# Optimization experiments

Measured on AMD Instinct MI355X. Metric: run time of the kernel, lower is better.

The kernel has to match this reference:

```python
import jax, jax.numpy as jnp
import numpy as np

B, T, H, NH = 2, 2048, 1024, 16
D = H // NH          # head dim = 64
K_CONV = 4           # short conv kernel size


def _dwconv_silu(x, w):
    # causal depthwise conv1d + silu; x:[B,T,C], w:[C,K]
    Kc = w.shape[1]
    xp = jnp.pad(x, ((0, 0), (Kc - 1, 0), (0, 0))).transpose(0, 2, 1)  # [B,C,T+K-1]
    y = jax.lax.conv_general_dilated(xp, w[:, None, :], (1,), 'VALID',
                                     feature_group_count=w.shape[0],
                                     dimension_numbers=('NCH', 'OIH', 'NCH'))
    return jax.nn.silu(y.transpose(0, 2, 1))


def _l2norm(x, eps=1e-6):
    return x * jax.lax.rsqrt(jnp.sum(x * x, -1, keepdims=True) + eps)


def _forward(hidden, Wq, Wk, Wv, conv_q, conv_k, conv_v, Wb, Wa, A_log, dt_bias, Wg, norm_w, Wo):
    Bh, Tt, Hh = hidden.shape
    nh = A_log.shape[0]
    d = Hh // nh
    q = _dwconv_silu(hidden @ Wq.T, conv_q).reshape(Bh, Tt, nh, d)
    k = _dwconv_silu(hidden @ Wk.T, conv_k).reshape(Bh, Tt, nh, d)
    v = _dwconv_silu(hidden @ Wv.T, conv_v).reshape(Bh, Tt, nh, d)
    q = _l2norm(q) * (d ** -0.5)
    k = _l2norm(k)
    beta = jax.nn.sigmoid(hidden @ Wb.T)                                  # [B,T,h]
    g = -jnp.exp(A_log) * jax.nn.softplus(hidden @ Wa.T + dt_bias)        # [B,T,h]

    def step(S, inp):
        qt, kt, vt, gt, bt = inp
        S = S * jnp.exp(gt)[..., None, None]                 # gated decay
        pred = jnp.einsum('bhk,bhkv->bhv', kt, S)            # current memory readout
        dv = (vt - pred) * bt[..., None]                     # delta-rule update
        S = S + jnp.einsum('bhk,bhv->bhkv', kt, dv)
        ot = jnp.einsum('bhk,bhkv->bhv', qt, S)
        return S, ot

    xs = (q.transpose(1, 0, 2, 3), k.transpose(1, 0, 2, 3), v.transpose(1, 0, 2, 3),
          g.transpose(1, 0, 2), beta.transpose(1, 0, 2))
    S0 = jnp.zeros((Bh, nh, d, d), hidden.dtype)
    _, o = jax.lax.scan(step, S0, xs)
    o = o.transpose(1, 0, 2, 3)                               # [B,T,h,d]
    gate = (hidden @ Wg.T).reshape(Bh, Tt, nh, d)
    o = o * jax.lax.rsqrt(jnp.mean(o * o, -1, keepdims=True) + 1e-5) * norm_w
    o = o * jax.nn.silu(gate)                                 # gated RMSNorm
    return o.reshape(Bh, Tt, Hh) @ Wo.T


def setup_inputs():
    key = jax.random.key(0)
    ks = jax.random.split(key, 16)
    s = 0.02
    return {
        'hidden': jax.random.normal(ks[0], (B, T, H), jnp.float32),
        'Wq': jax.random.normal(ks[1], (H, H), jnp.float32) * s,
        'Wk': jax.random.normal(ks[2], (H, H), jnp.float32) * s,
        'Wv': jax.random.normal(ks[3], (H, H), jnp.float32) * s,
        'conv_q': jax.random.normal(ks[4], (H, K_CONV), jnp.float32) * 0.5,
        'conv_k': jax.random.normal(ks[5], (H, K_CONV), jnp.float32) * 0.5,
        'conv_v': jax.random.normal(ks[6], (H, K_CONV), jnp.float32) * 0.5,
        'Wb': jax.random.normal(ks[7], (NH, H), jnp.float32) * s,
        'Wa': jax.random.normal(ks[8], (NH, H), jnp.float32) * s,
        'A_log': jnp.log(jax.random.uniform(ks[9], (NH,), jnp.float32, 1.0, 16.0)),
        'dt_bias': jnp.log(jnp.expm1(jax.random.uniform(ks[10], (NH,), jnp.float32, 1e-3, 0.1))),
        'Wg': jax.random.normal(ks[11], (H, H), jnp.float32) * s,
        'norm_w': jnp.ones((D,), jnp.float32),
        'Wo': jax.random.normal(ks[12], (H, H), jnp.float32) * s,
    }


def reference(hidden, Wq, Wk, Wv, conv_q, conv_k, conv_v, Wb, Wa, A_log, dt_bias, Wg, norm_w, Wo):
    return _forward(hidden, Wq, Wk, Wv, conv_q, conv_k, conv_v, Wb, Wa, A_log, dt_bias, Wg, norm_w, Wo)
```

## Files before the change

### kernel.cpp

```cpp
#include <hip/hip_runtime.h>
#include <hip/hip_bf16.h>

typedef unsigned short u16;
typedef __attribute__((ext_vector_type(4))) float f32x4;
typedef __attribute__((ext_vector_type(8))) short bf16x8;

#define TLEN 2048
#define NHEAD 16
#define HD 1024

__device__ inline u16 f2bf(float f) {
  unsigned x = __float_as_uint(f);
  return (u16)((x + 0x7fffu + ((x >> 16) & 1u)) >> 16);
}
__device__ inline float bf2f(u16 u) { return __uint_as_float(((unsigned)u) << 16); }

__device__ inline float wave_sum(float x) {
  x += __shfl_xor(x, 1);  x += __shfl_xor(x, 2);  x += __shfl_xor(x, 4);
  x += __shfl_xor(x, 8);  x += __shfl_xor(x, 16); x += __shfl_xor(x, 32);
  return x;
}

__device__ inline void storev(float* p, float v) { *p = v; }
__device__ inline void storev(u16* p, float v)   { *p = f2bf(v); }

__device__ inline int swz(int row, int col) {
  return (row << 7) + ((((col >> 3) ^ (row & 7)) << 4)) + ((col & 7) << 1);
}
__device__ inline bf16x8 frag(const u16* base, int row, int kslot) {
  return *(const bf16x8*)((const char*)base + (row << 7) +
                          (((kslot ^ (row & 7)) << 4)));
}

__global__ __launch_bounds__(256) void cvt_all(
    const float* __restrict__ h,  const float* __restrict__ wq,
    const float* __restrict__ wk, const float* __restrict__ wv,
    const float* __restrict__ wg, const float* __restrict__ wo,
    const float* __restrict__ Wb, const float* __restrict__ Wa,
    u16* __restrict__ dh,  u16* __restrict__ dhlo,
    u16* __restrict__ dwq, u16* __restrict__ dwk,
    u16* __restrict__ dwv, u16* __restrict__ dwg, u16* __restrict__ dwo,
    u16* __restrict__ dwba_h, u16* __restrict__ dwba_l) {
  const int b = blockIdx.x;
  if (b < 4096) {
    const size_t i = (size_t)b * 256 + threadIdx.x;
    float4 v = *(const float4*)(h + i * 4);
    ushort4 hi, lo;
    hi.x = f2bf(v.x); lo.x = f2bf(v.x - bf2f(hi.x));
    hi.y = f2bf(v.y); lo.y = f2bf(v.y - bf2f(hi.y));
    hi.z = f2bf(v.z); lo.z = f2bf(v.z - bf2f(hi.z));
    hi.w = f2bf(v.w); lo.w = f2bf(v.w - bf2f(hi.w));
    *(ushort4*)(dh + i * 4) = hi;
    *(ushort4*)(dhlo + i * 4) = lo;
  } else if (b < 9216) {
    const int wsel = (b - 4096) >> 10;
    const size_t i = (size_t)((b - 4096) & 1023) * 256 + threadIdx.x;
    const float* s; u16* d;
    switch (wsel) {
      case 0: s = wq; d = dwq; break;
      case 1: s = wk; d = dwk; break;
      case 2: s = wv; d = dwv; break;
      case 3: s = wg; d = dwg; break;
      default: s = wo; d = dwo; break;
    }
    float4 v = *(const float4*)(s + i * 4);
    ushort4 u;
    u.x = f2bf(v.x); u.y = f2bf(v.y); u.z = f2bf(v.z); u.w = f2bf(v.w);
    *(ushort4*)(d + i * 4) = u;
  } else {
    const size_t i = (size_t)(b - 9216) * 256 + threadIdx.x;
    const size_t flat = i * 4;
    const float* src = (flat < 16384) ? (Wb + flat) : (Wa + (flat - 16384));
    float4 v = *(const float4*)src;
    ushort4 hi, lo;
    hi.x = f2bf(v.x); lo.x = f2bf(v.x - bf2f(hi.x));
    hi.y = f2bf(v.y); lo.y = f2bf(v.y - bf2f(hi.y));
    hi.z = f2bf(v.z); lo.z = f2bf(v.z - bf2f(hi.z));
    hi.w = f2bf(v.w); lo.w = f2bf(v.w - bf2f(hi.w));
    *(ushort4*)(dwba_h + flat) = hi;
    *(ushort4*)(dwba_l + flat) = lo;
  }
}

__global__ __launch_bounds__(256, 2) void gemm_big(
    const u16* __restrict__ A,
    const u16* __restrict__ W0p, const u16* __restrict__ W1p,
    const u16* __restrict__ W2p, const u16* __restrict__ W3p,
    u16* __restrict__ C0, u16* __restrict__ C1,
    u16* __restrict__ C2, u16* __restrict__ C3,
    int M, int N, int K) {
  const u16* W; u16* C;
  switch (blockIdx.z) {
    case 0: W = W0p; C = C0; break;
    case 1: W = W1p; C = C1; break;
    case 2: W = W2p; C = C2; break;
    default: W = W3p; C = C3; break;
  }
  const int tid = threadIdx.x;
  const int lane = tid & 63, wid = tid >> 6;
  const int fr = lane & 15, fq = lane >> 4;
  const int row0 = blockIdx.y * 256, col0 = blockIdx.x * 128;
  __shared__ __align__(16) u16 As[256 * 64];
  __shared__ __align__(16) u16 Bs[128 * 64];

  const u16* aSrc[8]; const u16* bSrc[4];
#pragma unroll
  for (int it = 0; it < 8; ++it) {
    const int s = it * 256 + tid;
    const int r = s >> 3, cc = s & 7;
    aSrc[it] = A + (size_t)(row0 + r) * K + (cc ^ (r & 7)) * 8;
  }
#pragma unroll
  for (int it = 0; it < 4; ++it) {
    const int s = it * 256 + tid;
    const int r = s >> 3, cc = s & 7;
    bSrc[it] = W + (size_t)(col0 + r) * K + (cc ^ (r & 7)) * 8;
  }
  int aOff[4][2], bOff[8][2];
#pragma unroll
  for (int m = 0; m < 4; ++m)
#pragma unroll
    for (int kk = 0; kk < 2; ++kk) {
      const int ra = wid * 64 + m * 16 + fr;
      aOff[m][kk] = ra * 128 + ((((kk << 2) | fq) ^ (ra & 7)) << 4);
    }
#pragma unroll
  for (int n = 0; n < 8; ++n)
#pragma unroll
    for (int kk = 0; kk < 2; ++kk) {
      const int rb = n * 16 + fr;
      bOff[n][kk] = rb * 128 + ((((kk << 2) | fq) ^ (rb & 7)) << 4);
    }

  f32x4 acc[4][8] = {};
  for (int k0 = 0; k0 < K; k0 += 64) {
#pragma unroll
    for (int it = 0; it < 8; ++it)
      __builtin_amdgcn_global_load_lds(
          (const __attribute__((address_space(1))) void*)(aSrc[it] + k0),
          (__attribute__((address_space(3))) void*)((char*)As + (it * 256 + tid) * 16),
          16, 0, 0);
#pragma unroll
    for (int it = 0; it < 4; ++it)
      __builtin_amdgcn_global_load_lds(
          (const __attribute__((address_space(1))) void*)(bSrc[it] + k0),
          (__attribute__((address_space(3))) void*)((char*)Bs + (it * 256 + tid) * 16),
          16, 0, 0);
    __syncthreads();
#pragma unroll
    for (int kk = 0; kk < 2; ++kk) {
      bf16x8 af[4], bfr[8];
#pragma unroll
      for (int m = 0; m < 4; ++m)
        af[m] = *(const bf16x8*)((const char*)As + aOff[m][kk]);
#pragma unroll
      for (int n = 0; n < 8; ++n)
        bfr[n] = *(const bf16x8*)((const char*)Bs + bOff[n][kk]);
#pragma unroll
      for (int m = 0; m < 4; ++m)
#pragma unroll
        for (int n = 0; n < 8; ++n)
          acc[m][n] = __builtin_amdgcn_mfma_f32_16x16x32_bf16(af[m], bfr[n], acc[m][n], 0, 0, 0);
    }
    __syncthreads();
  }
#pragma unroll
  for (int m = 0; m < 4; ++m)
#pragma unroll
    for (int n = 0; n < 8; ++n)
#pragma unroll
      for (int r = 0; r < 4; ++r) {
        const int gr = row0 + wid * 64 + m * 16 + fq * 4 + r;
        const int gc = col0 + n * 16 + fr;
        C[(size_t)gr * N + gc] = f2bf(acc[m][n][r]);
      }
}

template <typename OutT, int MT>
__global__ __launch_bounds__(256) void gemm_lin(
    const u16* __restrict__ A, const u16* __restrict__ W,
    OutT* __restrict__ C, int M, int N, int K) {
  const int tid = threadIdx.x;
  const int lane = tid & 63, wid = tid >> 6;
  const int wr = wid >> 1, wc = wid & 1;
  const int fr = lane & 15, fq = lane >> 4;
  const int row0 = blockIdx.y * (MT * 32), col0 = blockIdx.x * 128;
  __shared__ __align__(16) u16 As[MT * 32 * 64];
  __shared__ __align__(16) u16 Bs[128 * 64];

  const u16* aSrc[MT]; const u16* bSrc[4];
#pragma unroll
  for (int it = 0; it < MT; ++it) {
    const int c = it * 256 + tid;
    const int r = c >> 3, cc = c & 7, sc = cc ^ (r & 7);
    aSrc[it] = A + (size_t)(row0 + r) * K + sc * 8;
  }
#pragma unroll
  for (int it = 0; it < 4; ++it) {
    const int c = it * 256 + tid;
    const int r = c >> 3, cc = c & 7, sc = cc ^ (r & 7);
    bSrc[it] = W + (size_t)(col0 + r) * K + sc * 8;
  }
  int aOff[MT][2], bOff[4][2];
#pragma unroll
  for (int m = 0; m < MT; ++m)
#pragma unroll
    for (int kk = 0; kk < 2; ++kk) {
      const int ra = wr * (MT * 16) + m * 16 + fr;
      aOff[m][kk] = ra * 128 + ((((kk << 2) | fq) ^ (fr & 7)) << 4);
    }
#pragma unroll
  for (int n = 0; n < 4; ++n)
#pragma unroll
    for (int kk = 0; kk < 2; ++kk) {
      const int rb = wc * 64 + n * 16 + fr;
      bOff[n][kk] = rb * 128 + ((((kk << 2) | fq) ^ (fr & 7)) << 4);
    }

  f32x4 acc[MT][4] = {};
  for (int k0 = 0; k0 < K; k0 += 64) {
#pragma unroll
    for (int it = 0; it < MT; ++it)
      __builtin_amdgcn_global_load_lds(
          (const __attribute__((address_space(1))) void*)(aSrc[it] + k0),
          (__attribute__((address_space(3))) void*)((char*)As + (it * 256 + wid * 64) * 16),
          16, 0, 0);
#pragma unroll
    for (int it = 0; it < 4; ++it)
      __builtin_amdgcn_global_load_lds(
          (const __attribute__((address_space(1))) void*)(bSrc[it] + k0),
          (__attribute__((address_space(3))) void*)((char*)Bs + (it * 256 + wid * 64) * 16),
          16, 0, 0);
    __syncthreads();
#pragma unroll
    for (int kk = 0; kk < 2; ++kk) {
      bf16x8 af[MT], bfr[4];
#pragma unroll
      for (int m = 0; m < MT; ++m)
        af[m] = *(const bf16x8*)((const char*)As + aOff[m][kk]);
#pragma unroll
      for (int n = 0; n < 4; ++n)
        bfr[n] = *(const bf16x8*)((const char*)Bs + bOff[n][kk]);
#pragma unroll
      for (int m = 0; m < MT; ++m)
#pragma unroll
        for (int n = 0; n < 4; ++n)
          acc[m][n] = __builtin_amdgcn_mfma_f32_16x16x32_bf16(af[m], bfr[n], acc[m][n], 0, 0, 0);
    }
    __syncthreads();
  }
#pragma unroll
  for (int m = 0; m < MT; ++m)
#pragma unroll
    for (int n = 0; n < 4; ++n)
#pragma unroll
      for (int r = 0; r < 4; ++r) {
        const int gr = row0 + wr * (MT * 16) + m * 16 + fq * 4 + r;
        const int gc = col0 + wc * 64 + n * 16 + fr;
        storev(&C[(size_t)gr * N + gc], acc[m][n][r]);
      }
}

__global__ __launch_bounds__(256) void small_mfma(
    const u16* __restrict__ hhi, const u16* __restrict__ hlo,
    const u16* __restrict__ whi, const u16* __restrict__ wlo,
    const float* __restrict__ A_log, const float* __restrict__ dtb,
    float* __restrict__ bbuf, float* __restrict__ gbuf) {
  extern __shared__ char smc[];
  u16* Ahi = (u16*)smc;
  u16* Alo = (u16*)(smc + 32768);
  float* Red = (float*)(smc + 65536);
  const int tid = threadIdx.x;
  const int row0 = blockIdx.x * 16;
#pragma unroll
  for (int i = 0; i < 8; ++i) {
    const int slot = tid + 256 * i;
    const int r = slot >> 7, s = slot & 127;
    const int ss = s ^ (r & 7);
    const size_t src = (size_t)(row0 + r) * 1024 + (size_t)ss * 8;
    __builtin_amdgcn_global_load_lds(
        (const __attribute__((address_space(1))) void*)(hhi + src),
        (__attribute__((address_space(3))) void*)(Ahi + (size_t)slot * 8), 16, 0, 0);
    __builtin_amdgcn_global_load_lds(
        (const __attribute__((address_space(1))) void*)(hlo + src),
        (__attribute__((address_space(3))) void*)(Alo + (size_t)slot * 8), 16, 0, 0);
  }
  __syncthreads();
  const int w = tid >> 6, lane = tid & 63, fr = lane & 15, fq = lane >> 4;
  f32x4 acc[2] = {};
#pragma unroll
  for (int kk = 0; kk < 8; ++kk) {
    const int s = w * 32 + kk * 4 + fq;
    const size_t k = (size_t)w * 256 + kk * 32 + fq * 8;
    const int aoff = ((fr << 7) + (s ^ (fr & 7))) * 8;
    bf16x8 ah = *(const bf16x8*)(Ahi + aoff);
    bf16x8 al = *(const bf16x8*)(Alo + aoff);
#pragma unroll
    for (int ct = 0; ct < 2; ++ct) {
      const size_t boff = (size_t)(ct * 16 + fr) * 1024 + k;
      bf16x8 bh = *(const bf16x8*)(whi + boff);
      bf16x8 bl = *(const bf16x8*)(wlo + boff);
      acc[ct] = __builtin_amdgcn_mfma_f32_16x16x32_bf16(ah, bh, acc[ct], 0, 0, 0);
      acc[ct] = __builtin_amdgcn_mfma_f32_16x16x32_bf16(ah, bl, acc[ct], 0, 0, 0);
      acc[ct] = __builtin_amdgcn_mfma_f32_16x16x32_bf16(al, bh, acc[ct], 0, 0, 0);
    }
  }
#pragma unroll
  for (int ct = 0; ct < 2; ++ct)
#pragma unroll
    for (int rr = 0; rr < 4; ++rr)
      Red[(w * 16 + fq * 4 + rr) * 33 + ct * 16 + fr] = acc[ct][rr];
  __syncthreads();
  if (tid < 128) {
    const int row = tid >> 3, cg = (tid & 7) * 4;
#pragma unroll
    for (int j = 0; j < 4; ++j) {
      const int col = cg + j;
      const float s = Red[(0 * 16 + row) * 33 + col] + Red[(1 * 16 + row) * 33 + col]
                    + Red[(2 * 16 + row) * 33 + col] + Red[(3 * 16 + row) * 33 + col];
      const int grow = row0 + row;
      if (col < 16) {
        bbuf[grow * NHEAD + col] = 1.f / (1.f + __expf(-s));
      } else {
        const int hh = col - 16;
        const float xs = s + dtb[hh];
        const float sp = (xs > 20.f) ? xs : log1pf(__expf(xs));
        gbuf[grow * NHEAD + hh] = -__expf(A_log[hh]) * sp;
      }
    }
  }
}

__global__ __launch_bounds__(256) void chunk_local(
    const u16* __restrict__ qp, const u16* __restrict__ kp, const u16* __restrict__ vp,
    const float* __restrict__ cq, const float* __restrict__ ck, const float* __restrict__ cv,
    const float* __restrict__ gbuf, const float* __restrict__ bbuf,
    float* __restrict__ Pg, u16* __restrict__ Ug,
    u16* __restrict__ Rg, u16* __restrict__ Yg) {
  __shared__ __align__(16) u16 Kb[64 * 64];
  __shared__ __align__(16) u16 Qb[64 * 64];
  __shared__ __align__(16) u16 K2T[64 * 64];
  __shared__ __align__(16) u16 KWt[64 * 64];
  __shared__ __align__(16) u16 Vt[64 * 64];
  __shared__ __align__(16) u16 Zb[64 * 64];
  __shared__ __align__(16) u16 Zt[64 * 64];
  __shared__ __align__(16) u16 Mb[64 * 72];
  __shared__ __align__(16) float Cb[16 * 64];
  __shared__ float bcs[64], bet[64], e2v[64], Bv[64];
  u16* WTh = Mb;
  u16* uTh = KWt;
  u16* Gb  = Vt;

  const int bid = blockIdx.x;
  const int c = bid & 31, bh = bid >> 5;
  const int b = bh >> 4, h = bh & 15;
  const int tid = threadIdx.x;

  {
    int* zp = (int*)Zt;
#pragma unroll
    for (int i = 0; i < 8; ++i) zp[tid + 256 * i] = 0;
  }
  if (tid < 64) {
    const size_t gi = (size_t)((b * TLEN + c * 64) + tid) * NHEAD + h;
    bet[tid] = bbuf[gi];
    float v = gbuf[gi];
#pragma unroll
    for (int ofs = 1; ofs < 64; ofs <<= 1) {
      float tt = __shfl_up(v, ofs);
      if (tid >= ofs) v += tt;
    }
    bcs[tid] = v;
  }
  __syncthreads();
  if (tid < 64) {
    const float blast = bcs[63];
    Bv[tid]  = __expf(bcs[tid]);
    e2v[tid] = __expf(blast - bcs[tid]);
  }
  __syncthreads();

  {
    const int dq = (tid & 15) * 4;
    const int col = h * 64 + dq;
    float4 wq4[4], wk4[4], wv4[4];
#pragma unroll
    for (int jj = 0; jj < 4; ++jj) {
      wq4[jj] = *(const float4*)(cq + (size_t)(col + jj) * 4);
      wk4[jj] = *(const float4*)(ck + (size_t)(col + jj) * 4);
      wv4[jj] = *(const float4*)(cv + (size_t)(col + jj) * 4);
    }
#pragma unroll
    for (int i = 0; i < 4; ++i) {
      const int r = i * 16 + (tid >> 4);
      const int tcur = c * 64 + r;
      ushort4 xq[4], xk[4], xv[4];
#pragma unroll
      for (int m = 0; m < 4; ++m) {
        const int tt = tcur - 3 + m;
        if (tt >= 0) {
          const size_t a = (size_t)(b * TLEN + tt) * HD + col;
          xq[m] = *(const ushort4*)(qp + a);
          xk[m] = *(const ushort4*)(kp + a);
          xv[m] = *(const ushort4*)(vp + a);
        } else {
          xq[m] = ushort4{0, 0, 0, 0}; xk[m] = xq[m]; xv[m] = xq[m];
        }
      }
      float yq[4], yk[4], yv[4];
      float ssq = 0.f, ssk = 0.f;
#pragma unroll
      for (int jj = 0; jj < 4; ++jj) {
        float aq = wq4[jj].x * bf2f(((const u16*)&xq[0])[jj]) +
                   wq4[jj].y * bf2f(((const u16*)&xq[1])[jj]) +
                   wq4[jj].z * bf2f(((const u16*)&xq[2])[jj]) +
                   wq4[jj].w * bf2f(((const u16*)&xq[3])[jj]);
        float ak = wk4[jj].x * bf2f(((const u16*)&xk[0])[jj]) +
                   wk4[jj].y * bf2f(((const u16*)&xk[1])[jj]) +
                   wk4[jj].z * bf2f(((const u16*)&xk[2])[jj]) +
                   wk4[jj].w * bf2f(((const u16*)&xk[3])[jj]);
        float av = wv4[jj].x * bf2f(((const u16*)&xv[0])[jj]) +
                   wv4[jj].y * bf2f(((const u16*)&xv[1])[jj]) +
                   wv4[jj].z * bf2f(((const u16*)&xv[2])[jj]) +
                   wv4[jj].w * bf2f(((const u16*)&xv[3])[jj]);
        yq[jj] = aq / (1.f + __expf(-aq));
        yk[jj] = ak / (1.f + __expf(-ak));
        yv[jj] = av / (1.f + __expf(-av));
        ssq += yq[jj] * yq[jj];
        ssk += yk[jj] * yk[jj];
      }
      ssq += __shfl_xor(ssq, 1); ssq += __shfl_xor(ssq, 2);
      ssq += __shfl_xor(ssq, 4); ssq += __shfl_xor(ssq, 8);
      ssk += __shfl_xor(ssk, 1); ssk += __shfl_xor(ssk, 2);
      ssk += __shfl_xor(ssk, 4); ssk += __shfl_xor(ssk, 8);
      const float qsc = rsqrtf(ssq + 1e-6f) * 0.125f;
      const float ksc = rsqrtf(ssk + 1e-6f);
      const float bR = bet[r], e2R = e2v[r], wscR = bR * Bv[r];
      ushort4 qo, ko;
      float kvf[4];
#pragma unroll
      for (int jj = 0; jj < 4; ++jj) kvf[jj] = yk[jj] * ksc;
      qo.x = f2bf(yq[0] * qsc); qo.y = f2bf(yq[1] * qsc);
      qo.z = f2bf(yq[2] * qsc); qo.w = f2bf(yq[3] * qsc);
      ko.x = f2bf(kvf[0]); ko.y = f2bf(kvf[1]);
      ko.z = f2bf(kvf[2]); ko.w = f2bf(kvf[3]);
      *(ushort4*)((char*)Qb + swz(r, dq)) = qo;
      *(ushort4*)((char*)Kb + swz(r, dq)) = ko;
#pragma unroll
      for (int jj = 0; jj < 4; ++jj) {
        *(u16*)((char*)K2T + swz(dq + jj, r)) = f2bf(kvf[jj] * e2R);
        *(u16*)((char*)KWt + swz(dq + jj, r)) = f2bf(kvf[jj] * wscR);
        *(u16*)((char*)Vt  + swz(dq + jj, r)) = f2bf(yv[jj] * bR);
      }
    }
  }
  __syncthreads();

  const int w = tid >> 6, lane = tid & 63, fr = lane & 15, fq = lane >> 4;
  {
    bf16x8 ka0 = frag(Kb, w * 16 + fr, fq);
    bf16x8 ka1 = frag(Kb, w * 16 + fr, 4 + fq);
#pragma unroll
    for (int tc = 0; tc < 4; ++tc) {
      bf16x8 kb0 = frag(Kb, tc * 16 + fr, fq);
      bf16x8 kb1 = frag(Kb, tc * 16 + fr, 4 + fq);
      f32x4 a = {};
      a = __builtin_amdgcn_mfma_f32_16x16x32_bf16(ka0, kb0, a, 0, 0, 0);
      a = __builtin_amdgcn_mfma_f32_16x16x32_bf16(ka1, kb1, a, 0, 0, 0);
#pragma unroll
      for (int rr = 0; rr < 4; ++rr) {
        const int t = w * 16 + fq * 4 + rr, s = tc * 16 + fr;
        const float mv = (s < t) ? bet[t] * __expf(bcs[t] - bcs[s]) * a[rr] : 0.f;
        Mb[t * 72 + s] = f2bf(mv);
      }
    }
  }
  __syncthreads();

#pragma unroll 1
  for (int bi = 0; bi < 4; ++bi) {
    {
      const char* mrow = (const char*)Mb + (size_t)(bi * 16 + fr) * 144;
      bf16x8 ma0 = *(const bf16x8*)(mrow + fq * 16);
      bf16x8 ma1 = *(const bf16x8*)(mrow + 64 + fq * 16);
      bf16x8 zt0 = frag(Zt, w * 16 + fr, fq);
      bf16x8 zt1 = frag(Zt, w * 16 + fr, 4 + fq);
      f32x4 a = {};
      a = __builtin_amdgcn_mfma_f32_16x16x32_bf16(ma0, zt0, a, 0, 0, 0);
      a = __builtin_amdgcn_mfma_f32_16x16x32_bf16(ma1, zt1, a, 0, 0, 0);
#pragma unroll
      for (int rr = 0; rr < 4; ++rr)
        Cb[(fq * 4 + rr) * 64 + w * 16 + fr] = a[rr];
    }
    __syncthreads();
    if (tid < 64) {
      const int j = tid;
      float z[16];
#pragma unroll
      for (int t = 0; t < 16; ++t) {
        float acc = ((bi * 16 + t) == j ? 1.f : 0.f) - Cb[t * 64 + j];
        const u16* mrow = Mb + (size_t)(bi * 16 + t) * 72 + bi * 16;
#pragma unroll
        for (int s = 0; s < t; ++s) acc -= bf2f(mrow[s]) * z[s];
        z[t] = acc;
      }
#pragma unroll
      for (int t = 0; t < 16; ++t)
        *(u16*)((char*)Zb + swz(bi * 16 + t, j)) = f2bf(z[t]);
#pragma unroll
      for (int t4 = 0; t4 < 4; ++t4) {
        ushort4 zz;
        zz.x = f2bf(z[t4 * 4 + 0]); zz.y = f2bf(z[t4 * 4 + 1]);
        zz.z = f2bf(z[t4 * 4 + 2]); zz.w = f2bf(z[t4 * 4 + 3]);
        *(ushort4*)((char*)Zt + swz(j, bi * 16 + t4 * 4)) = zz;
      }
    }
    __syncthreads();
  }

  f32x4 accW[4], accu[4], accG[4];
  {
    bf16x8 kw0 = frag(KWt, w * 16 + fr, fq), kw1 = frag(KWt, w * 16 + fr, 4 + fq);
    bf16x8 vt0 = frag(Vt,  w * 16 + fr, fq), vt1 = frag(Vt,  w * 16 + fr, 4 + fq);
    bf16x8 qa0 = frag(Qb,  w * 16 + fr, fq), qa1 = frag(Qb,  w * 16 + fr, 4 + fq);
#pragma unroll
    for (int tc = 0; tc < 4; ++tc) {
      bf16x8 z0 = frag(Zb, tc * 16 + fr, fq), z1 = frag(Zb, tc * 16 + fr, 4 + fq);
      bf16x8 kb0 = frag(Kb, tc * 16 + fr, fq), kb1 = frag(Kb, tc * 16 + fr, 4 + fq);
      f32x4 aw = {}, au = {}, ag = {};
      aw = __builtin_amdgcn_mfma_f32_16x16x32_bf16(kw0, z0, aw, 0, 0, 0);
      aw = __builtin_amdgcn_mfma_f32_16x16x32_bf16(kw1, z1, aw, 0, 0, 0);
      au = __builtin_amdgcn_mfma_f32_16x16x32_bf16(vt0, z0, au, 0, 0, 0);
      au = __builtin_amdgcn_mfma_f32_16x16x32_bf16(vt1, z1, au, 0, 0, 0);
      ag = __builtin_amdgcn_mfma_f32_16x16x32_bf16(qa0, kb0, ag, 0, 0, 0);
      ag = __builtin_amdgcn_mfma_f32_16x16x32_bf16(qa1, kb1, ag, 0, 0, 0);
      accW[tc] = aw; accu[tc] = au; accG[tc] = ag;
    }
  }
  __syncthreads();
#pragma unroll
  for (int tc = 0; tc < 4; ++tc)
#pragma unroll
    for (int rr = 0; rr < 4; ++rr) {
      const int ro = w * 16 + fq * 4 + rr, co = tc * 16 + fr;
      *(u16*)((char*)WTh + swz(ro, co)) = f2bf(accW[tc][rr]);
      *(u16*)((char*)uTh + swz(ro, co)) = f2bf(accu[tc][rr]);
      const float gv = (co <= ro) ? accG[tc][rr] * __expf(bcs[ro] - bcs[co]) : 0.f;
      *(u16*)((char*)Gb + swz(ro, co)) = f2bf(gv);
    }
  __syncthreads();

  {
    bf16x8 k20 = frag(K2T, w * 16 + fr, fq), k21 = frag(K2T, w * 16 + fr, 4 + fq);
    bf16x8 g0  = frag(Gb,  w * 16 + fr, fq), g1  = frag(Gb,  w * 16 + fr, 4 + fq);
    const float bl = Bv[63];
    const size_t off = (size_t)bid * 4096;
#pragma unroll
    for (int tc = 0; tc < 4; ++tc) {
      bf16x8 w0 = frag(WTh, tc * 16 + fr, fq), w1 = frag(WTh, tc * 16 + fr, 4 + fq);
      bf16x8 u0 = frag(uTh, tc * 16 + fr, fq), u1 = frag(uTh, tc * 16 + fr, 4 + fq);
      f32x4 aP = {}, aU = {}, aR = {}, aY = {};
      aP = __builtin_amdgcn_mfma_f32_16x16x32_bf16(k20, w0, aP, 0, 0, 0);
      aP = __builtin_amdgcn_mfma_f32_16x16x32_bf16(k21, w1, aP, 0, 0, 0);
      aU = __builtin_amdgcn_mfma_f32_16x16x32_bf16(k20, u0, aU, 0, 0, 0);
      aU = __builtin_amdgcn_mfma_f32_16x16x32_bf16(k21, u1, aU, 0, 0, 0);
      aR = __builtin_amdgcn_mfma_f32_16x16x32_bf16(g0, w0, aR, 0, 0, 0);
      aR = __builtin_amdgcn_mfma_f32_16x16x32_bf16(g1, w1, aR, 0, 0, 0);
      aY = __builtin_amdgcn_mfma_f32_16x16x32_bf16(g0, u0, aY, 0, 0, 0);
      aY = __builtin_amdgcn_mfma_f32_16x16x32_bf16(g1, u1, aY, 0, 0, 0);
#pragma unroll
      for (int rr = 0; rr < 4; ++rr) {
        const int ar = w * 16 + fq * 4 + rr, cb = tc * 16 + fr;
        Pg[off + ar * 64 + cb] = ((ar == cb) ? bl : 0.f) - aP[rr];
        Ug[off + ar * 64 + cb] = f2bf(aU[rr]);
        const float qv = bf2f(*(const u16*)((const char*)Qb + swz(ar, cb)));
        Rg[off + ar * 64 + cb] = f2bf(Bv[ar] * qv - aR[rr]);
        Yg[off + ar * 64 + cb] = f2bf(aY[rr]);
      }
    }
  }
}

__global__ __launch_bounds__(256) void state_step(
    const float* __restrict__ Pg, const u16* __restrict__ Ug,
    u16* __restrict__ Sst) {
  __shared__ float Ps[64 * 65];
  __shared__ float Sc[64 * 20];
  const int blk = blockIdx.x;
  const int bh = blk >> 2, j0 = (blk & 3) * 16;
  const int tid = threadIdx.x;
  const int a = tid >> 2, jb = (tid & 3) * 4;
  const int pr = tid >> 4, pc = (tid & 15) * 4;
  for (int i = tid; i < 64 * 20; i += 256) Sc[i] = 0.f;
  float4 pre[4];
  {
    const size_t off0 = (size_t)bh * 32 * 4096;
#pragma unroll
    for (int i = 0; i < 4; ++i)
      pre[i] = *(const float4*)(Pg + off0 + (size_t)(i * 16 + pr) * 64 + pc);
  }
  __syncthreads();
  for (int c = 0; c < 32; ++c) {
    const size_t off = ((size_t)bh * 32 + c) * 4096;
#pragma unroll
    for (int i = 0; i < 4; ++i) {
      float* dst = &Ps[(i * 16 + pr) * 65 + pc];
      dst[0] = pre[i].x; dst[1] = pre[i].y; dst[2] = pre[i].z; dst[3] = pre[i].w;
    }
    __syncthreads();
    if (c + 1 < 32) {
      const size_t offn = off + 4096;
#pragma unroll
      for (int i = 0; i < 4; ++i)
        pre[i] = *(const float4*)(Pg + offn + (size_t)(i * 16 + pr) * 64 + pc);
    }
    const float4 sc4 = *(const float4*)(&Sc[a * 20 + jb]);
    ushort4 so;
    so.x = f2bf(sc4.x); so.y = f2bf(sc4.y); so.z = f2bf(sc4.z); so.w = f2bf(sc4.w);
    *(ushort4*)(Sst + off + (size_t)a * 64 + j0 + jb) = so;
    const ushort4 uv = *(const ushort4*)(Ug + off + (size_t)a * 64 + j0 + jb);
    float4 acc;
    acc.x = bf2f(uv.x); acc.y = bf2f(uv.y); acc.z = bf2f(uv.z); acc.w = bf2f(uv.w);
    for (int k = 0; k < 64; ++k) {
      const float pv = Ps[a * 65 + k];
      const float4 sv = *(const float4*)(&Sc[k * 20 + jb]);
      acc.x += pv * sv.x; acc.y += pv * sv.y;
      acc.z += pv * sv.z; acc.w += pv * sv.w;
    }
    __syncthreads();
    *(float4*)(&Sc[a * 20 + jb]) = acc;
    __syncthreads();
  }
}

__global__ __launch_bounds__(256) void chunk_out(
    const u16* __restrict__ Rg, const u16* __restrict__ Yg,
    const u16* __restrict__ Sst, const u16* __restrict__ gatep,
    const float* __restrict__ norm_w, u16* __restrict__ outb) {
  __shared__ float Rs[64 * 65];
  __shared__ float Ss[64 * 65];
  const int bid = blockIdx.x;
  const int c = bid & 31, bh = bid >> 5, b = bh >> 4, h = bh & 15;
  const int tid = threadIdx.x;
  const size_t off = (size_t)bid * 4096;
#pragma unroll
  for (int i = 0; i < 2; ++i) {
    const int idx = i * 2048 + tid * 8;
    const int row = idx >> 6, col = idx & 63;
    const ushort4 r0 = *(const ushort4*)(Rg + off + idx);
    const ushort4 r1 = *(const ushort4*)(Rg + off + idx + 4);
    const ushort4 s0 = *(const ushort4*)(Sst + off + idx);
    const ushort4 s1 = *(const ushort4*)(Sst + off + idx + 4);
    float* rd = &Rs[row * 65 + col];
    rd[0]=bf2f(r0.x); rd[1]=bf2f(r0.y); rd[2]=bf2f(r0.z); rd[3]=bf2f(r0.w);
    rd[4]=bf2f(r1.x); rd[5]=bf2f(r1.y); rd[6]=bf2f(r1.z); rd[7]=bf2f(r1.w);
    float* sd = &Ss[row * 65 + col];
    sd[0]=bf2f(s0.x); sd[1]=bf2f(s0.y); sd[2]=bf2f(s0.z); sd[3]=bf2f(s0.w);
    sd[4]=bf2f(s1.x); sd[5]=bf2f(s1.y); sd[6]=bf2f(s1.z); sd[7]=bf2f(s1.w);
  }
  __syncthreads();
  const int tr = tid >> 4, tc = tid & 15;
  float acc[4][4];
#pragma unroll
  for (int i = 0; i < 4; ++i) {
    const ushort4 y = *(const ushort4*)(Yg + off + (4*tr+i)*64 + 4*tc);
    acc[i][0] = bf2f(y.x); acc[i][1] = bf2f(y.y);
    acc[i][2] = bf2f(y.z); acc[i][3] = bf2f(y.w);
  }
  for (int k = 0; k < 64; ++k) {
    float r0 = Rs[(4*tr+0)*65+k], r1 = Rs[(4*tr+1)*65+k],
          r2 = Rs[(4*tr+2)*65+k], r3 = Rs[(4*tr+3)*65+k];
    float s0 = Ss[k*65+4*tc+0], s1 = Ss[k*65+4*tc+1],
          s2 = Ss[k*65+4*tc+2], s3 = Ss[k*65+4*tc+3];
    acc[0][0]+=r0*s0; acc[0][1]+=r0*s1; acc[0][2]+=r0*s2; acc[0][3]+=r0*s3;
    acc[1][0]+=r1*s0; acc[1][1]+=r1*s1; acc[1][2]+=r1*s2; acc[1][3]+=r1*s3;
    acc[2][0]+=r2*s0; acc[2][1]+=r2*s1; acc[2][2]+=r2*s2; acc[2][3]+=r2*s3;
    acc[3][0]+=r3*s0; acc[3][1]+=r3*s1; acc[3][2]+=r3*s2; acc[3][3]+=r3*s3;
  }
  const float4 nw4 = *(const float4*)(norm_w + 4 * tc);
  const size_t btbase = (size_t)(b * TLEN + c * 64);
#pragma unroll
  for (int i = 0; i < 4; ++i) {
    float rs = acc[i][0]*acc[i][0] + acc[i][1]*acc[i][1]
             + acc[i][2]*acc[i][2] + acc[i][3]*acc[i][3];
    rs += __shfl_xor(rs, 1); rs += __shfl_xor(rs, 2);
    rs += __shfl_xor(rs, 4); rs += __shfl_xor(rs, 8);
    const float inv = rsqrtf(rs * (1.0f / 64.0f) + 1e-5f);
    const int t = 4 * tr + i;
    const size_t goff = (btbase + t) * 1024 + h * 64 + 4 * tc;
    const ushort4 gv = *(const ushort4*)(gatep + goff);
    const float g0 = bf2f(gv.x), g1 = bf2f(gv.y), g2 = bf2f(gv.z), g3 = bf2f(gv.w);
    ushort4 ov;
    ov.x = f2bf(acc[i][0] * inv * nw4.x * (g0 / (1.f + __expf(-g0))));
    ov.y = f2bf(acc[i][1] * inv * nw4.y * (g1 / (1.f + __expf(-g1))));
    ov.z = f2bf(acc[i][2] * inv * nw4.z * (g2 / (1.f + __expf(-g2))));
    ov.w = f2bf(acc[i][3] * inv * nw4.w * (g3 / (1.f + __expf(-g3))));
    *(ushort4*)(outb + goff) = ov;
  }
}

extern "C" void kernel_launch(void* const* d_in, const int* in_sizes, int n_in,
                              void* d_out, int out_size, void* d_ws, size_t ws_size,
                              hipStream_t stream) {
  const float* hidden = (const float*)d_in[0];
  const float* Wq     = (const float*)d_in[1];
  const float* Wk     = (const float*)d_in[2];
  const float* Wv     = (const float*)d_in[3];
  const float* cq     = (const float*)d_in[4];
  const float* ck     = (const float*)d_in[5];
  const float* cv     = (const float*)d_in[6];
  const float* Wb     = (const float*)d_in[7];
  const float* Wa     = (const float*)d_in[8];
  const float* A_log  = (const float*)d_in[9];
  const float* dtb    = (const float*)d_in[10];
  const float* Wg     = (const float*)d_in[11];
  const float* nw     = (const float*)d_in[12];
  const float* Wo     = (const float*)d_in[13];

  char* p = (char*)d_ws;
  const size_t MB = 1u << 20;
  u16* h_bf = (u16*)(p + 0 * MB);
  u16* wq_b = (u16*)(p + 8 * MB);
  u16* wk_b = (u16*)(p + 10 * MB);
  u16* wv_b = (u16*)(p + 12 * MB);
  u16* wg_b = (u16*)(p + 14 * MB);
  float* Pg = (float*)(p + 0 * MB);
  u16* wo_b = (u16*)(p + 16 * MB);
  u16* qp_b = (u16*)(p + 18 * MB);
  u16* kp_b = (u16*)(p + 26 * MB);
  u16* vp_b = (u16*)(p + 34 * MB);
  u16* gp_b = (u16*)(p + 42 * MB);
  u16*   of_b = vp_b;
  float* gbuf = (float*)(p + 50 * MB);
  float* bbuf = (float*)(p + 50 * MB + 262144);
  u16* Ug  = (u16*)(p + 51 * MB);
  u16* Rg  = (u16*)(p + 59 * MB);
  u16* Yg  = (u16*)(p + 67 * MB);
  u16* Sst = (u16*)(p + 75 * MB);
  u16* hlo_b = (u16*)(p + 83 * MB);
  u16* wba_h = (u16*)(p + 91 * MB);
  u16* wba_l = (u16*)(p + 91 * MB + 65536);

  cvt_all<<<9248, 256, 0, stream>>>(hidden, Wq, Wk, Wv, Wg, Wo, Wb, Wa,
                                    h_bf, hlo_b, wq_b, wk_b, wv_b, wg_b, wo_b,
                                    wba_h, wba_l);

  gemm_big<<<dim3(8, 16, 4), 256, 0, stream>>>(
      h_bf, wq_b, wk_b, wv_b, wg_b, qp_b, kp_b, vp_b, gp_b, 4096, 1024, 1024);

  const int sm_lds = 65536 + 8448;
  hipFuncSetAttribute((const void*)small_mfma,
                      hipFuncAttributeMaxDynamicSharedMemorySize, sm_lds);
  small_mfma<<<256, 256, sm_lds, stream>>>(h_bf, hlo_b, wba_h, wba_l,
                                           A_log, dtb, bbuf, gbuf);

  chunk_local<<<1024, 256, 0, stream>>>(qp_b, kp_b, vp_b, cq, ck, cv,
                                        gbuf, bbuf, Pg, Ug, Rg, Yg);
  state_step<<<128, 256, 0, stream>>>(Pg, Ug, Sst);
  chunk_out<<<1024, 256, 0, stream>>>(Rg, Yg, Sst, gp_b, nw, of_b);

  gemm_lin<float, 2><<<dim3(8, 64, 1), 256, 0, stream>>>(
      of_b, wo_b, (float*)d_out, 4096, 1024, 1024);
}
```

Measured before the change: 181.7 us.

## Run chunk state recurrence on MFMA with split-bf16 hi/lo operands

The inter-chunk state scan now computes S_next = U + P·S on matrix cores, using three bf16 MFMAs (hi·hi, hi·lo, lo·hi) to approximate fp32 precision. chunk_local emits P as hi/lo bf16 pairs in place of fp32. State is double-buffered in swizzled LDS, and one block per head handles the full 64-wide state instead of four blocks each owning 16 columns. This cuts the per-step latency of the serial scalar FMA loop, at the cost of fewer blocks and slightly reduced precision.

```diff
diff --git a/kernel.cpp b/kernel.cpp
--- a/kernel.cpp
+++ b/kernel.cpp
@@ -14,12 +14,6 @@
   return (u16)((x + 0x7fffu + ((x >> 16) & 1u)) >> 16);
 }
 __device__ inline float bf2f(u16 u) { return __uint_as_float(((unsigned)u) << 16); }
-
-__device__ inline float wave_sum(float x) {
-  x += __shfl_xor(x, 1);  x += __shfl_xor(x, 2);  x += __shfl_xor(x, 4);
-  x += __shfl_xor(x, 8);  x += __shfl_xor(x, 16); x += __shfl_xor(x, 32);
-  return x;
-}
 
 __device__ inline void storev(float* p, float v) { *p = v; }
 __device__ inline void storev(u16* p, float v)   { *p = f2bf(v); }
@@ -335,7 +329,7 @@
     const u16* __restrict__ qp, const u16* __restrict__ kp, const u16* __restrict__ vp,
     const float* __restrict__ cq, const float* __restrict__ ck, const float* __restrict__ cv,
     const float* __restrict__ gbuf, const float* __restrict__ bbuf,
-    float* __restrict__ Pg, u16* __restrict__ Ug,
+    u16* __restrict__ Phi, u16* __restrict__ Plo, u16* __restrict__ Ug,
     u16* __restrict__ Rg, u16* __restrict__ Yg) {
   __shared__ __align__(16) u16 Kb[64 * 64];
   __shared__ __align__(16) u16 Qb[64 * 64];
@@ -571,7 +565,10 @@
 #pragma unroll
       for (int rr = 0; rr < 4; ++rr) {
         const int ar = w * 16 + fq * 4 + rr, cb = tc * 16 + fr;
-        Pg[off + ar * 64 + cb] = ((ar == cb) ? bl : 0.f) - aP[rr];
+        const float pv = ((ar == cb) ? bl : 0.f) - aP[rr];
+        const u16 phv = f2bf(pv);
+        Phi[off + ar * 64 + cb] = phv;
+        Plo[off + ar * 64 + cb] = f2bf(pv - bf2f(phv));
         Ug[off + ar * 64 + cb] = f2bf(aU[rr]);
         const float qv = bf2f(*(const u16*)((const char*)Qb + swz(ar, cb)));
         Rg[off + ar * 64 + cb] = f2bf(Bv[ar] * qv - aR[rr]);
@@ -582,53 +579,86 @@
 }
 
 __global__ __launch_bounds__(256) void state_step(
-    const float* __restrict__ Pg, const u16* __restrict__ Ug,
-    u16* __restrict__ Sst) {
-  __shared__ float Ps[64 * 65];
-  __shared__ float Sc[64 * 20];
-  const int blk = blockIdx.x;
-  const int bh = blk >> 2, j0 = (blk & 3) * 16;
+    const u16* __restrict__ Phi, const u16* __restrict__ Plo,
+    const u16* __restrict__ Ug, u16* __restrict__ Sst) {
+  __shared__ __align__(16) u16 Sth[2][64 * 64];
+  __shared__ __align__(16) u16 Stl[2][64 * 64];
+  const int bh = blockIdx.x;
   const int tid = threadIdx.x;
-  const int a = tid >> 2, jb = (tid & 3) * 4;
-  const int pr = tid >> 4, pc = (tid & 15) * 4;
-  for (int i = tid; i < 64 * 20; i += 256) Sc[i] = 0.f;
-  float4 pre[4];
+  const int w = tid >> 6, lane = tid & 63, fr = lane & 15, fq = lane >> 4;
+  const size_t bbase = (size_t)bh * 32 * 4096;
   {
-    const size_t off0 = (size_t)bh * 32 * 4096;
+    int* p0 = (int*)&Sth[0][0];
+    int* p1 = (int*)&Stl[0][0];
+#pragma unroll
+    for (int i = 0; i < 8; ++i) { p0[tid + 256 * i] = 0; p1[tid + 256 * i] = 0; }
+    const ushort4 z4 = {0, 0, 0, 0};
 #pragma unroll
     for (int i = 0; i < 4; ++i)
-      pre[i] = *(const float4*)(Pg + off0 + (size_t)(i * 16 + pr) * 64 + pc);
-  }
-  __syncthreads();
+      *(ushort4*)(Sst + bbase + (size_t)tid * 16 + i * 4) = z4;
+  }
+  bf16x8 ph[2], pl[2];
+  float uin[4][4];
+#pragma unroll
+  for (int kk = 0; kk < 2; ++kk) {
+    const size_t ao = bbase + (size_t)(w * 16 + fr) * 64 + (kk * 4 + fq) * 8;
+    ph[kk] = *(const bf16x8*)(Phi + ao);
+    pl[kk] = *(const bf16x8*)(Plo + ao);
+  }
+#pragma unroll
+  for (int tc = 0; tc < 4; ++tc)
+#pragma unroll
+    for (int rr = 0; rr < 4; ++rr)
+      uin[tc][rr] = bf2f(Ug[bbase + (size_t)(w * 16 + fq * 4 + rr) * 64 + tc * 16 + fr]);
+  __syncthreads();
+  int cur = 0;
   for (int c = 0; c < 32; ++c) {
-    const size_t off = ((size_t)bh * 32 + c) * 4096;
-#pragma unroll
-    for (int i = 0; i < 4; ++i) {
-      float* dst = &Ps[(i * 16 + pr) * 65 + pc];
-      dst[0] = pre[i].x; dst[1] = pre[i].y; dst[2] = pre[i].z; dst[3] = pre[i].w;
-    }
-    __syncthreads();
+    f32x4 acc[4];
+    bf16x8 phc[2] = {ph[0], ph[1]}, plc[2] = {pl[0], pl[1]};
+#pragma unroll
+    for (int tc = 0; tc < 4; ++tc)
+#pragma unroll
+      for (int rr = 0; rr < 4; ++rr) acc[tc][rr] = uin[tc][rr];
     if (c + 1 < 32) {
-      const size_t offn = off + 4096;
-#pragma unroll
-      for (int i = 0; i < 4; ++i)
-        pre[i] = *(const float4*)(Pg + offn + (size_t)(i * 16 + pr) * 64 + pc);
-    }
-    const float4 sc4 = *(const float4*)(&Sc[a * 20 + jb]);
-    ushort4 so;
-    so.x = f2bf(sc4.x); so.y = f2bf(sc4.y); so.z = f2bf(sc4.z); so.w = f2bf(sc4.w);
-    *(ushort4*)(Sst + off + (size_t)a * 64 + j0 + jb) = so;
-    const ushort4 uv = *(const ushort4*)(Ug + off + (size_t)a * 64 + j0 + jb);
-    float4 acc;
-    acc.x = bf2f(uv.x); acc.y = bf2f(uv.y); acc.z = bf2f(uv.z); acc.w = bf2f(uv.w);
-    for (int k = 0; k < 64; ++k) {
-      const float pv = Ps[a * 65 + k];
-      const float4 sv = *(const float4*)(&Sc[k * 20 + jb]);
-      acc.x += pv * sv.x; acc.y += pv * sv.y;
-      acc.z += pv * sv.z; acc.w += pv * sv.w;
-    }
-    __syncthreads();
-    *(float4*)(&Sc[a * 20 + jb]) = acc;
+      const size_t off = bbase + (size_t)(c + 1) * 4096;
+#pragma unroll
+      for (int kk = 0; kk < 2; ++kk) {
+        const size_t ao = off + (size_t)(w * 16 + fr) * 64 + (kk * 4 + fq) * 8;
+        ph[kk] = *(const bf16x8*)(Phi + ao);
+        pl[kk] = *(const bf16x8*)(Plo + ao);
+      }
+#pragma unroll
+      for (int tc = 0; tc < 4; ++tc)
+#pragma unroll
+        for (int rr = 0; rr < 4; ++rr)
+          uin[tc][rr] = bf2f(Ug[off + (size_t)(w * 16 + fq * 4 + rr) * 64 + tc * 16 + fr]);
+    }
+#pragma unroll
+    for (int tc = 0; tc < 4; ++tc) {
+#pragma unroll
+      for (int kk = 0; kk < 2; ++kk) {
+        bf16x8 sh = frag(&Sth[cur][0], tc * 16 + fr, kk * 4 + fq);
+        bf16x8 sl = frag(&Stl[cur][0], tc * 16 + fr, kk * 4 + fq);
+        acc[tc] = __builtin_amdgcn_mfma_f32_16x16x32_bf16(phc[kk], sh, acc[tc], 0, 0, 0);
+        acc[tc] = __builtin_amdgcn_mfma_f32_16x16x32_bf16(phc[kk], sl, acc[tc], 0, 0, 0);
+        acc[tc] = __builtin_amdgcn_mfma_f32_16x16x32_bf16(plc[kk], sh, acc[tc], 0, 0, 0);
+      }
+    }
+    const int nxt = cur ^ 1;
+    const size_t offn = bbase + (size_t)(c + 1) * 4096;
+#pragma unroll
+    for (int tc = 0; tc < 4; ++tc)
+#pragma unroll
+      for (int rr = 0; rr < 4; ++rr) {
+        const float v = acc[tc][rr];
+        const int row = w * 16 + fq * 4 + rr;
+        const int col = tc * 16 + fr;
+        const u16 hv = f2bf(v);
+        *(u16*)((char*)&Sth[nxt][0] + swz(col, row)) = hv;
+        *(u16*)((char*)&Stl[nxt][0] + swz(col, row)) = f2bf(v - bf2f(hv));
+        if (c + 1 < 32) Sst[offn + (size_t)row * 64 + col] = hv;
+      }
+    cur = nxt;
     __syncthreads();
   }
 }
@@ -724,7 +754,8 @@
   u16* wk_b = (u16*)(p + 10 * MB);
   u16* wv_b = (u16*)(p + 12 * MB);
   u16* wg_b = (u16*)(p + 14 * MB);
-  float* Pg = (float*)(p + 0 * MB);
+  u16* Phi = (u16*)(p + 0 * MB);
+  u16* Plo = (u16*)(p + 8 * MB);
   u16* wo_b = (u16*)(p + 16 * MB);
   u16* qp_b = (u16*)(p + 18 * MB);
   u16* kp_b = (u16*)(p + 26 * MB);
@@ -755,8 +786,8 @@
                                            A_log, dtb, bbuf, gbuf);
 
   chunk_local<<<1024, 256, 0, stream>>>(qp_b, kp_b, vp_b, cq, ck, cv,
-                                        gbuf, bbuf, Pg, Ug, Rg, Yg);
-  state_step<<<128, 256, 0, stream>>>(Pg, Ug, Sst);
+                                        gbuf, bbuf, Phi, Plo, Ug, Rg, Yg);
+  state_step<<<32, 256, 0, stream>>>(Phi, Plo, Ug, Sst);
   chunk_out<<<1024, 256, 0, stream>>>(Rg, Yg, Sst, gp_b, nw, of_b);
 
   gemm_lin<float, 2><<<dim3(8, 64, 1), 256, 0, stream>>>(
```

Measured after the change: 181.4 us. About the same (-0.2%).
